# Performance work log

Hardware: AMD Instinct MI355X
Metric: run time of the kernel (lower is better)

The kernel has to match this reference:

```python
import jax, jax.numpy as jnp
import numpy as np

TM, TK = 64, 64
M, K = 4096, 4096
N_BLOCKS = 1024
T_SHAPE = (1, 2048, K)


def _gelu_tanh(x):
    # Matches the Triton kernel's tanh-approx GELU:
    inner = 0.7978845608 * (x + 0.044715 * x * x * x)
    return x * 0.5 * (1.0 + jnp.tanh(inner))


def setup_inputs() -> dict:
    key = jax.random.key(0)
    k1, k2, k3, k4, k5 = jax.random.split(key, 5)
    x = jax.random.normal(k1, T_SHAPE, dtype=jnp.float32)
    values = jax.random.normal(k2, (N_BLOCKS, TM, TK), dtype=jnp.float32) * 0.02
    bias = jax.random.normal(k3, (M,), dtype=jnp.float32) * 0.02
    block_rows = jax.random.randint(k4, (N_BLOCKS,), 0, M // TM, dtype=jnp.int32)
    block_cols = jax.random.randint(k5, (N_BLOCKS,), 0, K // TK, dtype=jnp.int32)
    return {"x": x, "values": values, "bias": bias,
            "block_rows": block_rows, "block_cols": block_cols}


def reference(x, values, bias, block_rows, block_cols):
    # y = gelu(W_sparse @ x^T + bias[:, None])^T, W stored as 64x64 blocks.
    in_features = x.shape[-1]
    out_features = bias.shape[0]
    n_row_blocks = out_features // TM
    x_flat = x.reshape(-1, in_features)          # [T, K]
    T = x_flat.shape[0]
    xb = x_flat.reshape(T, in_features // TK, TK)  # [T, nKblk, TK]
    g = xb[:, block_cols, :]                     # [T, nb, TK] gather per block col
    # per-block small GEMM: values[n] @ g[t, n]^T -> [nb, T, TM]
    partial = jnp.einsum('nmk,tnk->ntm', values, g)
    # scatter-add block contributions into their output row blocks
    outb = jax.ops.segment_sum(partial, block_rows, num_segments=n_row_blocks)
    y = outb.transpose(1, 0, 2).reshape(T, out_features)  # [T, M]
    y = _gelu_tanh(y + bias[None, :])
    return y.reshape(x.shape[:-1] + (out_features,))
```

## Files before the change

### kernel.cpp

```cpp
#include <hip/hip_runtime.h>
#include <hip/hip_bf16.h>

#define K_DIM 4096
#define M_DIM 4096
#define T_DIM 2048
#define NB    1024
#define BT    128
#define LSTRIDE 64

typedef __attribute__((ext_vector_type(8))) short bf16x8;
typedef __attribute__((ext_vector_type(4))) float f32x4;

__device__ __forceinline__ unsigned short f2bf(float f) {
    unsigned int u = __builtin_bit_cast(unsigned int, f);
    unsigned int r = (u + 0x7FFFu + ((u >> 16) & 1u)) >> 16;
    return (unsigned short)r;
}

__device__ __forceinline__ void gld16(const void* g, void* l) {
    __builtin_amdgcn_global_load_lds(
        (const __attribute__((address_space(1))) unsigned int*)g,
        (__attribute__((address_space(3))) unsigned int*)l, 16, 0, 0);
}

#define XCHUNKS (T_DIM * K_DIM / 8)
#define VCHUNKS (NB * 64 * 64 / 8)
#define NPREP   ((XCHUNKS + VCHUNKS) / 256)

__global__ __launch_bounds__(256) void prep_kernel(
    const float* __restrict__ x, const float* __restrict__ values,
    unsigned short* __restrict__ xb2, unsigned short* __restrict__ vb,
    const int* __restrict__ brows, const int* __restrict__ bcols,
    int* __restrict__ counts, unsigned int* __restrict__ lists)
{
    __shared__ int scnt[64];
    const int blk = blockIdx.x;
    if (blk == NPREP) {
        const int tid = threadIdx.x;
        if (tid < 64) scnt[tid] = 0;
        __syncthreads();
        for (int n = tid; n < NB; n += 256) {
            const int r = brows[n];
            const int p = atomicAdd(&scnt[r], 1);
            if (p < LSTRIDE)
                lists[r * LSTRIDE + p] = (unsigned)n | ((unsigned)bcols[n] << 16);
        }
        __syncthreads();
        if (tid < 64) counts[tid] = scnt[tid] < LSTRIDE ? scnt[tid] : LSTRIDE;
        return;
    }
    const int id = blk * 256 + threadIdx.x;
    if (id < XCHUNKS) {
        const int t   = id >> 9;
        const int rem = id & 511;
        const int c   = rem >> 3;
        const int o   = rem & 7;
        const float4* p = (const float4*)(x + (size_t)t * K_DIM + c * 64 + o * 8);
        const float4 a = p[0], b = p[1];
        uint4 w;
        w.x = (unsigned)f2bf(a.x) | ((unsigned)f2bf(a.y) << 16);
        w.y = (unsigned)f2bf(a.z) | ((unsigned)f2bf(a.w) << 16);
        w.z = (unsigned)f2bf(b.x) | ((unsigned)f2bf(b.y) << 16);
        w.w = (unsigned)f2bf(b.z) | ((unsigned)f2bf(b.w) << 16);
        *(uint4*)(xb2 + ((size_t)c * T_DIM + t) * 64 + o * 8) = w;
    } else {
        const int i = id - XCHUNKS;
        const float4* p = (const float4*)(values + (size_t)i * 8);
        const float4 a = p[0], b = p[1];
        uint4 w;
        w.x = (unsigned)f2bf(a.x) | ((unsigned)f2bf(a.y) << 16);
        w.y = (unsigned)f2bf(a.z) | ((unsigned)f2bf(a.w) << 16);
        w.z = (unsigned)f2bf(b.x) | ((unsigned)f2bf(b.y) << 16);
        w.w = (unsigned)f2bf(b.z) | ((unsigned)f2bf(b.w) << 16);
        *(uint4*)(vb + (size_t)i * 8) = w;
    }
}

__global__ __launch_bounds__(256, 3) void fsl_main(
    const unsigned short* __restrict__ xb2, const unsigned short* __restrict__ vb,
    const float* __restrict__ bias, const int* __restrict__ counts,
    const unsigned int* __restrict__ lists, float* __restrict__ out)
{
    __shared__ __align__(16) unsigned char sA[3][BT * 128];

    const int b     = blockIdx.x;
    const int xcd   = b & 7;
    const int slot  = b >> 3;
    const int ttile = xcd * 2 + (slot >> 6);
    const int t0    = ttile * BT;
    const int r     = slot & 63;

    const int cnt = counts[r];
    const unsigned int* lst = lists + r * LSTRIDE;

    const int tid  = threadIdx.x;
    const int wave = tid >> 6;
    const int lane = tid & 63;
    const int lrow = lane & 15;
    const int lk16 = lane >> 4;

    f32x4 acc[8] = {};

    const int srr    = lane >> 3;
    const int scol16 = lane & 7;

    auto stageA = [&](int i, int buf) {
        const int c = (int)(lst[i] >> 16);
        const unsigned short* src = xb2 + ((size_t)c * T_DIM + t0) * 64;
#pragma unroll
        for (int ch = 0; ch < 4; ++ch) {
            const int rbase = wave * 32 + ch * 8;
            const int row   = rbase + srr;
            const int sc    = (scol16 ^ (row & 7)) * 8;
            gld16(src + (size_t)row * 64 + sc, &sA[buf][rbase * 128]);
        }
    };

    auto loadB = [&](int i, bf16x8& b0, bf16x8& b1) {
        const int n = (int)(lst[i] & 0xFFFF);
        const unsigned short* vp =
            vb + (size_t)n * 4096 + (wave * 16 + lrow) * 64 + lk16 * 8;
        b0 = *(const bf16x8*)(vp);
        b1 = *(const bf16x8*)(vp + 32);
    };

    auto compute = [&](int buf, bf16x8 b0, bf16x8 b1) {
#pragma unroll
        for (int ks = 0; ks < 2; ++ks) {
            bf16x8 afr[8];
#pragma unroll
            for (int tf = 0; tf < 8; ++tf) {
                const int trow = tf * 16 + lrow;
                int abyte = trow * 128 + (ks * 32 + lk16 * 8) * 2;
                abyte ^= (trow & 7) << 4;
                afr[tf] = *(const bf16x8*)(&sA[buf][abyte]);
            }
            const bf16x8 bb = ks ? b1 : b0;
#pragma unroll
            for (int tf = 0; tf < 8; ++tf)
                acc[tf] = __builtin_amdgcn_mfma_f32_16x16x32_bf16(
                    afr[tf], bb, acc[tf], 0, 0, 0);
        }
    };

    auto waitfor = [&](int j) {
        const int rem = cnt - 1 - j;
        if (rem >= 2)      asm volatile("s_waitcnt vmcnt(12)" ::: "memory");
        else if (rem == 1) asm volatile("s_waitcnt vmcnt(6)"  ::: "memory");
        else               asm volatile("s_waitcnt vmcnt(0)"  ::: "memory");
    };

    bf16x8 a0, a1, bb0, bb1, c0, c1;
    if (cnt > 0) { stageA(0, 0); loadB(0, a0, a1); }
    if (cnt > 1) { stageA(1, 1); loadB(1, bb0, bb1); }
    for (int i = 0; i < cnt; i += 3) {
        if (i + 2 < cnt) { stageA(i + 2, 2); loadB(i + 2, c0, c1); }
        waitfor(i);
        __builtin_amdgcn_s_barrier();
        compute(0, a0, a1);
        __builtin_amdgcn_s_barrier();
        if (i + 1 >= cnt) break;

        if (i + 3 < cnt) { stageA(i + 3, 0); loadB(i + 3, a0, a1); }
        waitfor(i + 1);
        __builtin_amdgcn_s_barrier();
        compute(1, bb0, bb1);
        __builtin_amdgcn_s_barrier();
        if (i + 2 >= cnt) break;

        if (i + 4 < cnt) { stageA(i + 4, 1); loadB(i + 4, bb0, bb1); }
        waitfor(i + 2);
        __builtin_amdgcn_s_barrier();
        compute(2, c0, c1);
        __builtin_amdgcn_s_barrier();
    }

    const int mg = r * 64 + wave * 16 + (lane & 15);
    const float bv = bias[mg];
    const int tbase = t0 + (lane >> 4) * 4;
#pragma unroll
    for (int tf = 0; tf < 8; ++tf) {
#pragma unroll
        for (int reg = 0; reg < 4; ++reg) {
            const int t = tbase + tf * 16 + reg;
            float v = acc[tf][reg] + bv;
            float inner = 0.7978845608f * (v + 0.044715f * v * v * v);
            inner = fminf(fmaxf(inner, -15.0f), 15.0f);
            const float e  = __expf(2.0f * inner);
            const float th = 1.0f - 2.0f / (e + 1.0f);
            out[(size_t)t * M_DIM + mg] = v * 0.5f * (1.0f + th);
        }
    }
}

__global__ __launch_bounds__(256, 2) void fsl_mfma_fallback(
    const float* __restrict__ x, const float* __restrict__ values,
    const float* __restrict__ bias, const int* __restrict__ brows,
    const int* __restrict__ bcols, float* __restrict__ out)
{
    __shared__ __align__(16) unsigned char sA[2][64 * 128];
    __shared__ __align__(16) unsigned char sB[2][64 * 128];
    __shared__ int s_list[NB];
    __shared__ int s_cnt;

    const int tid = threadIdx.x;
    const int r   = blockIdx.x >> 5;
    const int t0  = (blockIdx.x & 31) * 64;

    if (tid == 0) s_cnt = 0;
    __syncthreads();
    for (int n = tid; n < NB; n += 256) {
        if (brows[n] == r) {
            int p = atomicAdd(&s_cnt, 1);
            s_list[p] = n;
        }
    }
    __syncthreads();
    const int cnt = s_cnt;

    const int wave = tid >> 6;
    const int lane = tid & 63;
    const int wt   = wave >> 1;
    const int wm   = wave & 1;
    const int lrow = lane & 15;
    const int lk8  = (lane >> 4) * 8;
    const int srow = tid >> 4;
    const int scol = tid & 15;

    f32x4 acc[2][2] = {};
    float4 ra[4], rb[4];

    auto stage_load = [&](int i) {
        const int n = s_list[i];
        const int c = bcols[n];
        const float* xp = x + (size_t)(t0 + srow) * K_DIM + c * 64 + scol * 4;
        const float* vp = values + (size_t)n * 4096 + srow * 64 + scol * 4;
#pragma unroll
        for (int j = 0; j < 4; ++j) {
            ra[j] = *(const float4*)(xp + (size_t)(j * 16) * K_DIM);
            rb[j] = *(const float4*)(vp + j * 16 * 64);
        }
    };
    auto stage_write = [&](int buf) {
#pragma unroll
        for (int j = 0; j < 4; ++j) {
            const int row = srow + j * 16;
            int byte = row * 128 + scol * 8;
            byte ^= (row & 7) << 4;
            uint2 pa, pb;
            pa.x = (unsigned)f2bf(ra[j].x) | ((unsigned)f2bf(ra[j].y) << 16);
            pa.y = (unsigned)f2bf(ra[j].z) | ((unsigned)f2bf(ra[j].w) << 16);
            pb.x = (unsigned)f2bf(rb[j].x) | ((unsigned)f2bf(rb[j].y) << 16);
            pb.y = (unsigned)f2bf(rb[j].z) | ((unsigned)f2bf(rb[j].w) << 16);
            *(uint2*)(&sA[buf][byte]) = pa;
            *(uint2*)(&sB[buf][byte]) = pb;
        }
    };
    auto compute = [&](int buf) {
#pragma unroll
        for (int ks = 0; ks < 2; ++ks) {
            bf16x8 a[2], bb[2];
#pragma unroll
            for (int f = 0; f < 2; ++f) {
                const int trow = wt * 32 + f * 16 + lrow;
                int abyte = trow * 128 + (ks * 32 + lk8) * 2;
                abyte ^= (trow & 7) << 4;
                a[f] = *(const bf16x8*)(&sA[buf][abyte]);
                const int mrow = wm * 32 + f * 16 + lrow;
                int bbyte = mrow * 128 + (ks * 32 + lk8) * 2;
                bbyte ^= (mrow & 7) << 4;
                bb[f] = *(const bf16x8*)(&sB[buf][bbyte]);
            }
#pragma unroll
            for (int ft = 0; ft < 2; ++ft)
#pragma unroll
                for (int fm = 0; fm < 2; ++fm)
                    acc[ft][fm] = __builtin_amdgcn_mfma_f32_16x16x32_bf16(
                        a[ft], bb[fm], acc[ft][fm], 0, 0, 0);
        }
    };

    if (cnt > 0) { stage_load(0); stage_write(0); }
    for (int i = 0; i < cnt; ++i) {
        __syncthreads();
        const bool more = (i + 1 < cnt);
        if (more) stage_load(i + 1);
        compute(i & 1);
        if (more) stage_write((i + 1) & 1);
    }

    const int mcol  = lane & 15;
    const int trow4 = (lane >> 4) * 4;
#pragma unroll
    for (int ft = 0; ft < 2; ++ft) {
#pragma unroll
        for (int fm = 0; fm < 2; ++fm) {
            const int mg = r * 64 + wm * 32 + fm * 16 + mcol;
            const float bv = bias[mg];
#pragma unroll
            for (int reg = 0; reg < 4; ++reg) {
                const int t = t0 + wt * 32 + ft * 16 + trow4 + reg;
                float v = acc[ft][fm][reg] + bv;
                float inner = 0.7978845608f * (v + 0.044715f * v * v * v);
                inner = fminf(fmaxf(inner, -15.0f), 15.0f);
                const float e  = __expf(2.0f * inner);
                const float th = 1.0f - 2.0f / (e + 1.0f);
                out[(size_t)t * M_DIM + mg] = v * 0.5f * (1.0f + th);
            }
        }
    }
}

extern "C" void kernel_launch(void* const* d_in, const int* in_sizes, int n_in,
                              void* d_out, int out_size, void* d_ws, size_t ws_size,
                              hipStream_t stream) {
    const float* x      = (const float*)d_in[0];
    const float* values = (const float*)d_in[1];
    const float* bias   = (const float*)d_in[2];
    const int*   brows  = (const int*)d_in[3];
    const int*   bcols  = (const int*)d_in[4];
    float* out = (float*)d_out;

    const size_t x_elems = (size_t)T_DIM * K_DIM;
    const size_t v_elems = (size_t)NB * 64 * 64;
    const size_t sched_b = 64 * 4 + 64 * LSTRIDE * 4;
    const size_t ws_need = (x_elems + v_elems) * 2 + sched_b;

    if (ws_size >= ws_need) {
        unsigned short* xb2   = (unsigned short*)d_ws;
        unsigned short* vb    = xb2 + x_elems;
        int*            cnts  = (int*)(vb + v_elems);
        unsigned int*   lists = (unsigned int*)(cnts + 64);
        prep_kernel<<<NPREP + 1, 256, 0, stream>>>(x, values, xb2, vb,
                                                   brows, bcols, cnts, lists);
        fsl_main<<<dim3(1024), 256, 0, stream>>>(xb2, vb, bias, cnts, lists, out);
    } else {
        fsl_mfma_fallback<<<dim3(64 * 32), 256, 0, stream>>>(
            x, values, bias, brows, bcols, out);
    }
}
```

Baseline: 148.8 us.

## Repartition waves over token rows, double-buffer LDS, raise occupancy to four blocks

```diff
diff --git a/kernel.cpp b/kernel.cpp
--- a/kernel.cpp
+++ b/kernel.cpp
@@ -76,19 +76,19 @@
     }
 }
 
-__global__ __launch_bounds__(256, 3) void fsl_main(
+__global__ __launch_bounds__(256, 4) void fsl_main(
     const unsigned short* __restrict__ xb2, const unsigned short* __restrict__ vb,
     const float* __restrict__ bias, const int* __restrict__ counts,
     const unsigned int* __restrict__ lists, float* __restrict__ out)
 {
-    __shared__ __align__(16) unsigned char sA[3][BT * 128];
+    __shared__ __align__(16) unsigned char sA[2][BT * 128];
 
     const int b     = blockIdx.x;
     const int xcd   = b & 7;
     const int slot  = b >> 3;
-    const int ttile = xcd * 2 + (slot >> 6);
+    const int ttile = xcd * 2 + (slot & 1);
     const int t0    = ttile * BT;
-    const int r     = slot & 63;
+    const int r     = slot >> 1;
 
     const int cnt = counts[r];
     const unsigned int* lst = lists + r * LSTRIDE;
@@ -99,7 +99,7 @@
     const int lrow = lane & 15;
     const int lk16 = lane >> 4;
 
-    f32x4 acc[8] = {};
+    f32x4 acc[2][4] = {};
 
     const int srr    = lane >> 3;
     const int scol16 = lane & 7;
@@ -116,79 +116,78 @@
         }
     };
 
-    auto loadB = [&](int i, bf16x8& b0, bf16x8& b1) {
+    auto loadB = [&](int i, bf16x8* bf) {
         const int n = (int)(lst[i] & 0xFFFF);
-        const unsigned short* vp =
-            vb + (size_t)n * 4096 + (wave * 16 + lrow) * 64 + lk16 * 8;
-        b0 = *(const bf16x8*)(vp);
-        b1 = *(const bf16x8*)(vp + 32);
-    };
-
-    auto compute = [&](int buf, bf16x8 b0, bf16x8 b1) {
+        const unsigned short* base = vb + (size_t)n * 4096 + lrow * 64 + lk16 * 8;
+#pragma unroll
+        for (int ks = 0; ks < 2; ++ks)
+#pragma unroll
+            for (int fm = 0; fm < 4; ++fm)
+                bf[ks * 4 + fm] = *(const bf16x8*)(base + fm * 16 * 64 + ks * 32);
+    };
+
+    auto compute = [&](int buf, const bf16x8* bf) {
 #pragma unroll
         for (int ks = 0; ks < 2; ++ks) {
-            bf16x8 afr[8];
-#pragma unroll
-            for (int tf = 0; tf < 8; ++tf) {
-                const int trow = tf * 16 + lrow;
+            bf16x8 a[2];
+#pragma unroll
+            for (int tf = 0; tf < 2; ++tf) {
+                const int trow = wave * 32 + tf * 16 + lrow;
                 int abyte = trow * 128 + (ks * 32 + lk16 * 8) * 2;
                 abyte ^= (trow & 7) << 4;
-                afr[tf] = *(const bf16x8*)(&sA[buf][abyte]);
+                a[tf] = *(const bf16x8*)(&sA[buf][abyte]);
             }
-            const bf16x8 bb = ks ? b1 : b0;
-#pragma unroll
-            for (int tf = 0; tf < 8; ++tf)
-                acc[tf] = __builtin_amdgcn_mfma_f32_16x16x32_bf16(
-                    afr[tf], bb, acc[tf], 0, 0, 0);
-        }
-    };
-
-    auto waitfor = [&](int j) {
-        const int rem = cnt - 1 - j;
-        if (rem >= 2)      asm volatile("s_waitcnt vmcnt(12)" ::: "memory");
-        else if (rem == 1) asm volatile("s_waitcnt vmcnt(6)"  ::: "memory");
-        else               asm volatile("s_waitcnt vmcnt(0)"  ::: "memory");
-    };
-
-    bf16x8 a0, a1, bb0, bb1, c0, c1;
-    if (cnt > 0) { stageA(0, 0); loadB(0, a0, a1); }
-    if (cnt > 1) { stageA(1, 1); loadB(1, bb0, bb1); }
-    for (int i = 0; i < cnt; i += 3) {
-        if (i + 2 < cnt) { stageA(i + 2, 2); loadB(i + 2, c0, c1); }
-        waitfor(i);
+#pragma unroll
+            for (int tf = 0; tf < 2; ++tf)
+#pragma unroll
+                for (int fm = 0; fm < 4; ++fm)
+                    acc[tf][fm] = __builtin_amdgcn_mfma_f32_16x16x32_bf16(
+                        a[tf], bf[ks * 4 + fm], acc[tf][fm], 0, 0, 0);
+        }
+    };
+
+    bf16x8 be[8], bo[8];
+    if (cnt > 0) { stageA(0, 0); loadB(0, be); }
+    for (int i = 0; i < cnt; i += 2) {
+        if (i + 1 < cnt) {
+            stageA(i + 1, 1); loadB(i + 1, bo);
+            asm volatile("s_waitcnt vmcnt(12)" ::: "memory");
+        } else {
+            asm volatile("s_waitcnt vmcnt(0)" ::: "memory");
+        }
         __builtin_amdgcn_s_barrier();
-        compute(0, a0, a1);
+        compute(0, be);
         __builtin_amdgcn_s_barrier();
         if (i + 1 >= cnt) break;
 
-        if (i + 3 < cnt) { stageA(i + 3, 0); loadB(i + 3, a0, a1); }
-        waitfor(i + 1);
+        if (i + 2 < cnt) {
+            stageA(i + 2, 0); loadB(i + 2, be);
+            asm volatile("s_waitcnt vmcnt(12)" ::: "memory");
+        } else {
+            asm volatile("s_waitcnt vmcnt(0)" ::: "memory");
+        }
         __builtin_amdgcn_s_barrier();
-        compute(1, bb0, bb1);
+        compute(1, bo);
         __builtin_amdgcn_s_barrier();
-        if (i + 2 >= cnt) break;
-
-        if (i + 4 < cnt) { stageA(i + 4, 1); loadB(i + 4, bb0, bb1); }
-        waitfor(i + 2);
-        __builtin_amdgcn_s_barrier();
-        compute(2, c0, c1);
-        __builtin_amdgcn_s_barrier();
-    }
-
-    const int mg = r * 64 + wave * 16 + (lane & 15);
-    const float bv = bias[mg];
-    const int tbase = t0 + (lane >> 4) * 4;
-#pragma unroll
-    for (int tf = 0; tf < 8; ++tf) {
-#pragma unroll
-        for (int reg = 0; reg < 4; ++reg) {
-            const int t = tbase + tf * 16 + reg;
-            float v = acc[tf][reg] + bv;
-            float inner = 0.7978845608f * (v + 0.044715f * v * v * v);
-            inner = fminf(fmaxf(inner, -15.0f), 15.0f);
-            const float e  = __expf(2.0f * inner);
-            const float th = 1.0f - 2.0f / (e + 1.0f);
-            out[(size_t)t * M_DIM + mg] = v * 0.5f * (1.0f + th);
+    }
+
+    const int tbase = t0 + wave * 32 + (lane >> 4) * 4;
+#pragma unroll
+    for (int tf = 0; tf < 2; ++tf) {
+#pragma unroll
+        for (int fm = 0; fm < 4; ++fm) {
+            const int mg = r * 64 + fm * 16 + (lane & 15);
+            const float bv = bias[mg];
+#pragma unroll
+            for (int reg = 0; reg < 4; ++reg) {
+                const int t = tbase + tf * 16 + reg;
+                float v = acc[tf][fm][reg] + bv;
+                float inner = 0.7978845608f * (v + 0.044715f * v * v * v);
+                inner = fminf(fmaxf(inner, -15.0f), 15.0f);
+                const float e  = __expf(2.0f * inner);
+                const float th = 1.0f - 2.0f / (e + 1.0f);
+                out[(size_t)t * M_DIM + mg] = v * 0.5f * (1.0f + th);
+            }
         }
     }
 }
```

Measured after the change: 261.8 us. 1.76x slower.
